# Optimization experiments

Hardware: AMD Instinct MI355X
Metric: run time of the kernel (lower is better)

The kernel has to match this reference:

```python
import jax, jax.numpy as jnp
import numpy as np

B, C, E_OLD, U = 8, 128, 48000, 8000
E_NEW = E_OLD + 3 * U  # unroll_target = 72000


def setup_inputs() -> dict:
    key = jax.random.key(0)
    kf, kw, kp = jax.random.split(key, 3)
    features = jax.random.normal(kf, (B, C, E_OLD), dtype=jnp.float32)
    weights = jax.random.uniform(kw, (B, U, 2, 3), dtype=jnp.float32)
    # Per-mesh permutation of the unrolled edge slots -> disjoint index groups
    perms = jax.vmap(lambda k: jax.random.permutation(k, E_NEW))(
        jax.random.split(kp, B)
    ).astype(jnp.int32)
    old_idx = perms[:, :E_OLD]                      # slots of relocated old edges
    left_idx = old_idx[:, :U]                       # source edges of unpool events
    right_idx = old_idx[:, U:2 * U]
    new_block = perms[:, E_OLD:]                    # 3U brand-new slots
    new_idx = new_block[:, :U]
    new_left_idx = new_block[:, U:2 * U]
    new_right_idx = new_block[:, 2 * U:3 * U]
    return {
        "features": features,
        "weights": weights,
        "old_idx": old_idx,
        "left_idx": left_idx,
        "right_idx": right_idx,
        "new_idx": new_idx,
        "new_left_idx": new_left_idx,
        "new_right_idx": new_right_idx,
    }


def _unpool_one(feat, w, old_i, l_i, r_i, n_i, nl_i, nr_i):
    # feat: [C, E_OLD], w: [U, 2, 3]
    nf = jnp.zeros((feat.shape[0], E_NEW), feat.dtype).at[:, old_i].set(feat)
    lf = nf[:, l_i]                                 # [C, U] left source features
    rf = nf[:, r_i]                                 # [C, U]
    lw, rw = w[:, 0, :], w[:, 1, :]                 # [U, 3] each
    nf = nf.at[:, l_i].set(lf * lw[:, 0])
    nf = nf.at[:, nl_i].set(lf * lw[:, 1])
    nf = nf.at[:, r_i].set(rf * rw[:, 0])
    nf = nf.at[:, nr_i].set(rf * rw[:, 1])
    nf = nf.at[:, n_i].set((lf * lw[:, 2] + rf * rw[:, 2]) * 0.5)
    return nf


def reference(features, weights, old_idx, left_idx, right_idx, new_idx,
              new_left_idx, new_right_idx):
    return jax.vmap(_unpool_one)(features, weights, old_idx, left_idx,
                                 right_idx, new_idx, new_left_idx,
                                 new_right_idx)  # [B, C, E_NEW]
```

## Files before the change

kernel.cpp:

```cpp
#include <hip/hip_runtime.h>


constexpr int B_     = 8;
constexpr int C_     = 128;
constexpr int E_OLD_ = 48000;
constexpr int U_     = 8000;
constexpr int E_NEW_ = E_OLD_ + 3 * U_;
constexpr int T_PER_B = U_ + (E_OLD_ - 2 * U_);

__device__ __forceinline__ int4 pack_map(int s0, int s1, float w0, float w1) {
    return make_int4(s0, s1, __float_as_int(w0), __float_as_int(w1));
}

__global__ __launch_bounds__(256)
void build_map_kernel(const float* __restrict__ w,
                      const int*   __restrict__ old_idx,
                      const int*   __restrict__ new_idx,
                      const int*   __restrict__ new_left,
                      const int*   __restrict__ new_right,
                      int4*        __restrict__ map) {
    const int b = blockIdx.y;
    const int t = blockIdx.x * blockDim.x + threadIdx.x;
    if (t >= T_PER_B) return;

    int4* mb = map + (size_t)b * E_NEW_;

    if (t < U_) {
        const int u   = t;
        const int jl  = old_idx [b * E_OLD_ + u];
        const int jr  = old_idx [b * E_OLD_ + U_ + u];
        const int jn  = new_idx [b * U_ + u];
        const int jnl = new_left [b * U_ + u];
        const int jnr = new_right[b * U_ + u];

        const float* wp = w + ((size_t)b * U_ + u) * 6;
        const float lw0 = wp[0], lw1 = wp[1], lw2 = wp[2];
        const float rw0 = wp[3], rw1 = wp[4], rw2 = wp[5];

        mb[jl]  = pack_map(u,       u,       lw0,        0.f);
        mb[jnl] = pack_map(u,       u,       lw1,        0.f);
        mb[jr]  = pack_map(U_ + u,  U_ + u,  rw0,        0.f);
        mb[jnr] = pack_map(U_ + u,  U_ + u,  rw1,        0.f);
        mb[jn]  = pack_map(u,       U_ + u,  0.5f * lw2, 0.5f * rw2);
    } else {
        const int e = t + U_;
        const int j = old_idx[b * E_OLD_ + e];
        mb[j] = pack_map(e, e, 1.0f, 0.f);
    }
}

constexpr int TT = 32;

__global__ __launch_bounds__(256)
void transpose_kernel(const float* __restrict__ feat,
                      float*       __restrict__ featT,
                      int b0) {
    __shared__ float tile[TT][TT + 1];
    const int bl = blockIdx.z;
    const int b  = b0 + bl;
    const int e0 = blockIdx.x * TT;
    const int c0 = blockIdx.y * TT;
    const int tx = threadIdx.x;
    const int ty = threadIdx.y;

    const float* fb = feat + (size_t)b * C_ * E_OLD_;
    #pragma unroll
    for (int i = 0; i < 4; ++i) {
        const int c = c0 + ty + 8 * i;
        tile[ty + 8 * i][tx] = fb[(size_t)c * E_OLD_ + e0 + tx];
    }
    __syncthreads();
    float* ft = featT + (size_t)bl * E_OLD_ * C_;
    #pragma unroll
    for (int i = 0; i < 4; ++i) {
        const int e = e0 + ty + 8 * i;
        ft[(size_t)e * C_ + c0 + tx] = tile[tx][ty + 8 * i];
    }
}

constexpr int JT = 64;
constexpr int TILES_PER_B = E_NEW_ / JT;

__global__ __launch_bounds__(256)
void gatherT_kernel(const float* __restrict__ featT,
                    const int4*  __restrict__ map,
                    float*       __restrict__ out,
                    int b0, int nb) {
    __shared__ float tile[JT][C_ + 4];
    const int bl    = blockIdx.x % nb;
    const int b     = b0 + bl;
    const int chunk = blockIdx.x / nb;
    const int j0    = chunk * JT;
    const int t     = threadIdx.x;

    {
        const int j  = t >> 2;
        const int cq = t & 3;
        const int4 m = map[(size_t)b * E_NEW_ + j0 + j];
        const float w0 = __int_as_float(m.z);
        const float w1 = __int_as_float(m.w);

        const float* fTb = featT + (size_t)bl * E_OLD_ * C_;
        const float4* r0 = (const float4*)(fTb + (size_t)m.x * C_) + cq * 8;

        float4 acc[8];
        #pragma unroll
        for (int i = 0; i < 8; ++i) {
            const float4 f = r0[i];
            acc[i].x = w0 * f.x;
            acc[i].y = w0 * f.y;
            acc[i].z = w0 * f.z;
            acc[i].w = w0 * f.w;
        }
        if (w1 != 0.f) {
            const float4* r1 = (const float4*)(fTb + (size_t)m.y * C_) + cq * 8;
            #pragma unroll
            for (int i = 0; i < 8; ++i) {
                const float4 f = r1[i];
                acc[i].x += w1 * f.x;
                acc[i].y += w1 * f.y;
                acc[i].z += w1 * f.z;
                acc[i].w += w1 * f.w;
            }
        }
        float* trow = &tile[j][cq * 32];
        #pragma unroll
        for (int i = 0; i < 8; ++i) {
            *(float4*)(trow + 4 * i) = acc[i];
        }
    }
    __syncthreads();

    {
        const int j  = t & 63;
        const int cg = t >> 6;
        const float* trow = &tile[j][cg * 32];
        float* ob = out + (size_t)b * C_ * E_NEW_
                        + (size_t)(cg * 32) * E_NEW_ + j0 + j;
        #pragma unroll
        for (int k4 = 0; k4 < 8; ++k4) {
            const float4 v = *(const float4*)(trow + 4 * k4);
            ob[(size_t)(4 * k4 + 0) * E_NEW_] = v.x;
            ob[(size_t)(4 * k4 + 1) * E_NEW_] = v.y;
            ob[(size_t)(4 * k4 + 2) * E_NEW_] = v.z;
            ob[(size_t)(4 * k4 + 3) * E_NEW_] = v.w;
        }
    }
}

constexpr int K2_BLOCK     = 256;
constexpr int CHUNKS_PER_B = (E_NEW_ + K2_BLOCK - 1) / K2_BLOCK;

__global__ __launch_bounds__(K2_BLOCK)
void gather_kernel(const float* __restrict__ feat,
                   const int4*  __restrict__ map,
                   float*       __restrict__ out) {
    const int b     = blockIdx.x % B_;
    const int chunk = blockIdx.x / B_;
    const int j     = chunk * K2_BLOCK + threadIdx.x;
    if (j >= E_NEW_) return;

    const int4 m  = map[(size_t)b * E_NEW_ + j];
    const int  s0 = m.x;
    const int  s1 = m.y;
    const float w0 = __int_as_float(m.z);
    const float w1 = __int_as_float(m.w);

    const float* fb = feat + (size_t)b * C_ * E_OLD_;
    float*       ob = out  + (size_t)b * C_ * E_NEW_ + j;

    #pragma unroll 4
    for (int c = 0; c < C_; ++c) {
        const float f0 = fb[s0];
        const float f1 = fb[s1];
        *ob = w0 * f0 + w1 * f1;
        fb += E_OLD_;
        ob += E_NEW_;
    }
}

extern "C" void kernel_launch(void* const* d_in, const int* in_sizes, int n_in,
                              void* d_out, int out_size, void* d_ws, size_t ws_size,
                              hipStream_t stream) {
    const float* feat      = (const float*)d_in[0];
    const float* w         = (const float*)d_in[1];
    const int*   old_idx   = (const int*)  d_in[2];
    const int*   new_idx   = (const int*)  d_in[5];
    const int*   new_left  = (const int*)  d_in[6];
    const int*   new_right = (const int*)  d_in[7];
    float*       out       = (float*)d_out;

    int4* map = (int4*)d_ws;
    const size_t map_bytes = (size_t)B_ * E_NEW_ * sizeof(int4);
    const size_t featT_off = (map_bytes + 255) & ~(size_t)255;
    const size_t featT_one = (size_t)E_OLD_ * C_ * sizeof(float);
    const size_t featT_all = (size_t)B_ * featT_one;
    float* featT = (float*)((char*)d_ws + featT_off);

    {
        dim3 block(256);
        dim3 grid((T_PER_B + 255) / 256, B_);
        build_map_kernel<<<grid, block, 0, stream>>>(
            w, old_idx, new_idx, new_left, new_right, map);
    }

    if (ws_size >= featT_off + featT_all) {
        {
            dim3 block(32, 8);
            dim3 grid(E_OLD_ / TT, C_ / TT, B_);
            transpose_kernel<<<grid, block, 0, stream>>>(feat, featT, 0);
        }
        {
            dim3 block(256);
            dim3 grid(TILES_PER_B * B_);
            gatherT_kernel<<<grid, block, 0, stream>>>(featT, map, out, 0, B_);
        }
    } else if (ws_size >= featT_off + featT_one) {
        for (int b = 0; b < B_; ++b) {
            dim3 tblock(32, 8);
            dim3 tgrid(E_OLD_ / TT, C_ / TT, 1);
            transpose_kernel<<<tgrid, tblock, 0, stream>>>(feat, featT, b);
            dim3 gblock(256);
            dim3 ggrid(TILES_PER_B);
            gatherT_kernel<<<ggrid, gblock, 0, stream>>>(featT, map, out, b, 1);
        }
    } else {
        dim3 block(K2_BLOCK);
        dim3 grid(CHUNKS_PER_B * B_);
        gather_kernel<<<grid, block, 0, stream>>>(feat, map, out);
    }
}
```

Measured before the change: 549.9 us.

## Halve gather LDS tile with two-phase writeback, widen transpose tiles, nontemporal stores

The gather kernel's shared tile shrinks from 64x132 to 64x68 floats. Channels are now written back in two 64-channel halves with extra barriers, which lowers LDS per block so more blocks can be resident. Output stores become nontemporal so the large streamed output is less likely to pollute the cache. The transpose kernel moves to 64x64 tiles with a 1D 256-thread block, each thread moving 16 elements. The extra synchronisation and the changed LDS access strides could offset some of the occupancy benefit.

```diff
diff --git a/kernel.cpp b/kernel.cpp
--- a/kernel.cpp
+++ b/kernel.cpp
@@ -49,7 +49,7 @@
     }
 }
 
-constexpr int TT = 32;
+constexpr int TT = 64;
 
 __global__ __launch_bounds__(256)
 void transpose_kernel(const float* __restrict__ feat,
@@ -60,21 +60,23 @@
     const int b  = b0 + bl;
     const int e0 = blockIdx.x * TT;
     const int c0 = blockIdx.y * TT;
-    const int tx = threadIdx.x;
-    const int ty = threadIdx.y;
-
-    const float* fb = feat + (size_t)b * C_ * E_OLD_;
-    #pragma unroll
-    for (int i = 0; i < 4; ++i) {
-        const int c = c0 + ty + 8 * i;
-        tile[ty + 8 * i][tx] = fb[(size_t)c * E_OLD_ + e0 + tx];
+    const int t  = threadIdx.x;
+    const int lx = t & 63;
+    const int ly = t >> 6;
+
+    const float* fb = feat + (size_t)b * C_ * E_OLD_ + e0 + lx;
+    #pragma unroll
+    for (int i = 0; i < 16; ++i) {
+        const int cl = ly * 16 + i;
+        tile[cl][lx] = fb[(size_t)(c0 + cl) * E_OLD_];
     }
     __syncthreads();
-    float* ft = featT + (size_t)bl * E_OLD_ * C_;
-    #pragma unroll
-    for (int i = 0; i < 4; ++i) {
-        const int e = e0 + ty + 8 * i;
-        ft[(size_t)e * C_ + c0 + tx] = tile[tx][ty + 8 * i];
+
+    float* ft = featT + (size_t)bl * E_OLD_ * C_ + c0 + lx;
+    #pragma unroll
+    for (int i = 0; i < 16; ++i) {
+        const int el = ly * 16 + i;
+        ft[(size_t)(e0 + el) * C_] = tile[lx][el];
     }
 }
 
@@ -86,65 +88,65 @@
                     const int4*  __restrict__ map,
                     float*       __restrict__ out,
                     int b0, int nb) {
-    __shared__ float tile[JT][C_ + 4];
+    __shared__ float tile[JT][68];
     const int bl    = blockIdx.x % nb;
     const int b     = b0 + bl;
     const int chunk = blockIdx.x / nb;
     const int j0    = chunk * JT;
     const int t     = threadIdx.x;
 
-    {
-        const int j  = t >> 2;
-        const int cq = t & 3;
-        const int4 m = map[(size_t)b * E_NEW_ + j0 + j];
-        const float w0 = __int_as_float(m.z);
-        const float w1 = __int_as_float(m.w);
-
-        const float* fTb = featT + (size_t)bl * E_OLD_ * C_;
-        const float4* r0 = (const float4*)(fTb + (size_t)m.x * C_) + cq * 8;
-
-        float4 acc[8];
+    const int j  = t >> 2;
+    const int cq = t & 3;
+
+    const int4 m = map[(size_t)b * E_NEW_ + j0 + j];
+    const float w0 = __int_as_float(m.z);
+    const float w1 = __int_as_float(m.w);
+
+    const float* fTb = featT + (size_t)bl * E_OLD_ * C_;
+    const float4* r0 = (const float4*)(fTb + (size_t)m.x * C_) + cq * 8;
+
+    float4 acc[8];
+    #pragma unroll
+    for (int i = 0; i < 8; ++i) {
+        const float4 f = r0[i];
+        acc[i].x = w0 * f.x;
+        acc[i].y = w0 * f.y;
+        acc[i].z = w0 * f.z;
+        acc[i].w = w0 * f.w;
+    }
+    if (w1 != 0.f) {
+        const float4* r1 = (const float4*)(fTb + (size_t)m.y * C_) + cq * 8;
         #pragma unroll
         for (int i = 0; i < 8; ++i) {
-            const float4 f = r0[i];
-            acc[i].x = w0 * f.x;
-            acc[i].y = w0 * f.y;
-            acc[i].z = w0 * f.z;
-            acc[i].w = w0 * f.w;
-        }
-        if (w1 != 0.f) {
-            const float4* r1 = (const float4*)(fTb + (size_t)m.y * C_) + cq * 8;
+            const float4 f = r1[i];
+            acc[i].x += w1 * f.x;
+            acc[i].y += w1 * f.y;
+            acc[i].z += w1 * f.z;
+            acc[i].w += w1 * f.w;
+        }
+    }
+
+    const int jj = t & 63;
+    const int q  = t >> 6;
+
+    #pragma unroll
+    for (int h = 0; h < 2; ++h) {
+        if ((cq >> 1) == h) {
+            float* trow = &tile[j][(cq & 1) * 32];
             #pragma unroll
-            for (int i = 0; i < 8; ++i) {
-                const float4 f = r1[i];
-                acc[i].x += w1 * f.x;
-                acc[i].y += w1 * f.y;
-                acc[i].z += w1 * f.z;
-                acc[i].w += w1 * f.w;
-            }
-        }
-        float* trow = &tile[j][cq * 32];
-        #pragma unroll
-        for (int i = 0; i < 8; ++i) {
-            *(float4*)(trow + 4 * i) = acc[i];
-        }
-    }
-    __syncthreads();
-
-    {
-        const int j  = t & 63;
-        const int cg = t >> 6;
-        const float* trow = &tile[j][cg * 32];
-        float* ob = out + (size_t)b * C_ * E_NEW_
-                        + (size_t)(cg * 32) * E_NEW_ + j0 + j;
-        #pragma unroll
-        for (int k4 = 0; k4 < 8; ++k4) {
-            const float4 v = *(const float4*)(trow + 4 * k4);
-            ob[(size_t)(4 * k4 + 0) * E_NEW_] = v.x;
-            ob[(size_t)(4 * k4 + 1) * E_NEW_] = v.y;
-            ob[(size_t)(4 * k4 + 2) * E_NEW_] = v.z;
-            ob[(size_t)(4 * k4 + 3) * E_NEW_] = v.w;
-        }
+            for (int i = 0; i < 8; ++i)
+                *(float4*)(trow + 4 * i) = acc[i];
+        }
+        __syncthreads();
+        {
+            const float* tr = &tile[jj][q * 16];
+            float* ob = out + (size_t)b * C_ * E_NEW_
+                            + (size_t)(h * 64 + q * 16) * E_NEW_ + j0 + jj;
+            #pragma unroll
+            for (int k = 0; k < 16; ++k)
+                __builtin_nontemporal_store(tr[k], ob + (size_t)k * E_NEW_);
+        }
+        if (h == 0) __syncthreads();
     }
 }
 
@@ -206,7 +208,7 @@
 
     if (ws_size >= featT_off + featT_all) {
         {
-            dim3 block(32, 8);
+            dim3 block(256);
             dim3 grid(E_OLD_ / TT, C_ / TT, B_);
             transpose_kernel<<<grid, block, 0, stream>>>(feat, featT, 0);
         }
@@ -217,7 +219,7 @@
         }
     } else if (ws_size >= featT_off + featT_one) {
         for (int b = 0; b < B_; ++b) {
-            dim3 tblock(32, 8);
+            dim3 tblock(256);
             dim3 tgrid(E_OLD_ / TT, C_ / TT, 1);
             transpose_kernel<<<tgrid, tblock, 0, stream>>>(feat, featT, b);
             dim3 gblock(256);
```

After: 566.9 us. +3.1%, slower.
